# Optimization experiments

Measured on AMD Instinct MI355X. Metric: run time of the kernel, lower is better.

The kernel has to match this reference:

```python
import jax, jax.numpy as jnp
import numpy as np

B = 2048        # graphs per batch
NC = 81         # cells per sudoku
IN_C, HID = 10, 128
N_ACT, N_NUM, N_TECH = 4, 9, 10


def _sudoku_edges():
    idx = np.arange(NC).reshape(9, 9)
    adj = np.zeros((NC, NC), dtype=bool)
    for i in range(9):
        for j in range(9):
            n = idx[i, j]
            adj[n, idx[i, :]] = True
            adj[n, idx[:, j]] = True
            bi, bj = 3 * (i // 3), 3 * (j // 3)
            adj[n, idx[bi:bi + 3, bj:bj + 3].reshape(-1)] = True
            adj[n, n] = False
    src, dst = np.nonzero(adj)  # 1620 directed edges
    return np.stack([src, dst]).astype(np.int32)


def setup_inputs() -> dict:
    key = jax.random.key(0)
    ks = jax.random.split(key, 12)
    N = B * NC
    base = _sudoku_edges()                          # [2, 1620]
    offs = (np.arange(B, dtype=np.int32) * NC)      # [B]
    ei = (base[:, None, :] + offs[None, :, None]).reshape(2, -1)  # [2, B*1620]
    batch = np.repeat(np.arange(B, dtype=np.int32), NC)           # [N]

    def lin(k, fan_in, fan_out):
        s = 1.0 / np.sqrt(fan_in)
        return jax.random.uniform(k, (fan_in, fan_out), jnp.float32, -s, s)

    return {
        "x": jax.random.normal(ks[0], (N, IN_C), jnp.float32),
        "edge_index": jnp.asarray(ei),
        "batch": jnp.asarray(batch),
        "W1": lin(ks[1], IN_C, HID), "b1": jnp.zeros((HID,), jnp.float32),
        "W2": lin(ks[2], HID, HID),  "b2": jnp.zeros((HID,), jnp.float32),
        "Wa": lin(ks[3], HID, N_ACT),  "ba": jnp.zeros((N_ACT,), jnp.float32),
        "Wc": lin(ks[4], HID, NC),     "bc": jnp.zeros((NC,), jnp.float32),
        "Wn": lin(ks[5], HID, N_NUM),  "bn": jnp.zeros((N_NUM,), jnp.float32),
        "Wt": lin(ks[6], HID, N_TECH), "bt": jnp.zeros((N_TECH,), jnp.float32),
    }


def _gcn_conv(x, edge_index, W, b):
    n = x.shape[0]
    loop = jnp.arange(n, dtype=edge_index.dtype)
    src = jnp.concatenate([edge_index[0], loop])
    dst = jnp.concatenate([edge_index[1], loop])
    deg = jax.ops.segment_sum(jnp.ones_like(dst, jnp.float32), dst, num_segments=n)
    dinv = jax.lax.rsqrt(deg)            # deg >= 1 due to self-loops
    norm = dinv[src] * dinv[dst]         # [E+N]
    h = x @ W                            # [N, out]
    msg = h[src] * norm[:, None]         # gather + scale
    return jax.ops.segment_sum(msg, dst, num_segments=n) + b


def reference(x, edge_index, batch, W1, b1, W2, b2, Wa, ba, Wc, bc, Wn, bn, Wt, bt):
    h = jax.nn.relu(_gcn_conv(x, edge_index, W1, b1))
    h = jax.nn.relu(_gcn_conv(h, edge_index, W2, b2))
    # global mean pool over graphs
    sums = jax.ops.segment_sum(h, batch, num_segments=B)
    cnts = jax.ops.segment_sum(jnp.ones((h.shape[0],), h.dtype), batch, num_segments=B)
    pooled = sums / jnp.maximum(cnts, 1.0)[:, None]   # [B, HID]
    return (pooled @ Wa + ba, pooled @ Wc + bc, pooled @ Wn + bn, pooled @ Wt + bt)
```

## Files before the change

### kernel.cpp

```cpp
#include <hip/hip_runtime.h>
#include <hip/hip_bf16.h>

typedef __attribute__((ext_vector_type(8))) short bf16x8;
typedef __attribute__((ext_vector_type(4))) float f32x4;

__device__ __forceinline__ unsigned short f2b(float f) {
    __hip_bfloat16 h = __float2bfloat16(f);
    return __builtin_bit_cast(unsigned short, h);
}
__device__ __forceinline__ float b2f(unsigned short u) {
    unsigned v = ((unsigned)u) << 16;
    return __builtin_bit_cast(float, v);
}
__device__ __forceinline__ float ldf(const void* p, int idx, bool f32) {
    return f32 ? ((const float*)p)[idx] : b2f(((const unsigned short*)p)[idx]);
}
__device__ __forceinline__ unsigned short ldb(const void* p, int idx, bool f32) {
    return f32 ? f2b(((const float*)p)[idx]) : ((const unsigned short*)p)[idx];
}
__device__ __forceinline__ int swz(int row, int col) {
    return row * 128 + (((col >> 3) ^ (row & 7)) << 3) + (col & 7);
}

__device__ __forceinline__ bool sniff_f32(const void* x) {
    const unsigned* p = (const unsigned*)x;
    int wild = 0;
#pragma unroll
    for (int i = 0; i < 16; ++i) {
        unsigned e = (p[i] >> 7) & 0xFF;
        wild += (e != 0 && (e < 0x68 || e > 0x90)) ? 1 : 0;
    }
    return wild > 8;
}

#define WS_B1F    16
#define WS_B2F    528
#define WS_BHF    1040
#define WS_W1R    1536
#define WS_W2R    9728
#define WS_SR     42496
#define WS_WH     60928

__global__ void k_repack(const void* __restrict__ x,
                         const void* __restrict__ W1, const void* __restrict__ b1,
                         const void* __restrict__ W2, const void* __restrict__ b2,
                         const void* __restrict__ Wa, const void* __restrict__ ba,
                         const void* __restrict__ Wc, const void* __restrict__ bc,
                         const void* __restrict__ Wn, const void* __restrict__ bn,
                         const void* __restrict__ Wt, const void* __restrict__ bt,
                         char* __restrict__ ws) {
    const bool f32 = sniff_f32(x);
    int idx = blockIdx.x * blockDim.x + threadIdx.x;
    if (idx < 4096) {
        int f = idx >> 5, k = idx & 31;
        unsigned short v = (k < 10) ? ldb(W1, k * 128 + f, f32) : (unsigned short)0;
        ((unsigned short*)(ws + WS_W1R))[idx] = v;
        return;
    }
    idx -= 4096;
    if (idx < 16384) {
        int f = idx >> 7, k = idx & 127;
        ((unsigned short*)(ws + WS_W2R))[idx] = ldb(W2, k * 128 + f, f32);
        return;
    }
    idx -= 16384;
    if (idx < 9216) {
        int fi = idx >> 9, rem = idx & 511;
        int lane = rem >> 3, j = rem & 7;
        int mi = fi / 3, kc = fi - mi * 3;
        int node = mi * 16 + (lane & 15);
        int cell = kc * 32 + ((lane >> 4) << 3) + j;
        bool adj = false;
        if (node < 81 && cell < 81) {
            int ni = node / 9, nj = node % 9;
            int ci = cell / 9, cj = cell % 9;
            adj = (ni == ci) || (nj == cj) ||
                  ((ni / 3 == ci / 3) && (nj / 3 == cj / 3));
        }
        ((unsigned short*)(ws + WS_SR))[idx] = adj ? (unsigned short)0x3F80 : (unsigned short)0;
        return;
    }
    idx -= 9216;
    if (idx < 13312) {
        int o = idx >> 7, f = idx & 127;
        const void* W; int oo, dim;
        if (o < 4)       { W = Wa; oo = o;      dim = 4;  }
        else if (o < 85) { W = Wc; oo = o - 4;  dim = 81; }
        else if (o < 94) { W = Wn; oo = o - 85; dim = 9;  }
        else             { W = Wt; oo = o - 94; dim = 10; }
        ((float*)(ws + WS_WH))[idx] = ldf(W, f * dim + oo, f32);
        return;
    }
    idx -= 13312;
    if (idx < 360) {
        float v;
        if (idx < 128)      v = ldf(b1, idx, f32);
        else if (idx < 256) v = ldf(b2, idx - 128, f32);
        else {
            int o = idx - 256;
            if (o < 4)       v = ldf(ba, o, f32);
            else if (o < 85) v = ldf(bc, o - 4, f32);
            else if (o < 94) v = ldf(bn, o - 85, f32);
            else             v = ldf(bt, o - 94, f32);
        }
        if (idx < 128)      ((float*)(ws + WS_B1F))[idx] = v;
        else if (idx < 256) ((float*)(ws + WS_B2F))[idx - 128] = v;
        else                ((float*)(ws + WS_BHF))[idx - 256] = v;
    }
}

__global__ __launch_bounds__(256, 2) void sudoku_gnn(
    const void* __restrict__ x, const char* __restrict__ ws,
    void* __restrict__ out, int nB)
{
    __shared__ __attribute__((aligned(16))) unsigned short tT[16384];
    __shared__ __attribute__((aligned(16))) unsigned short hS[12288];
    __shared__ float sPool[4][128];

    const bool f32 = sniff_f32(x);
    const unsigned short* w1r = (const unsigned short*)(ws + WS_W1R);
    const unsigned short* w2r = (const unsigned short*)(ws + WS_W2R);
    const unsigned short* sr  = (const unsigned short*)(ws + WS_SR);
    const float* b1f = (const float*)(ws + WS_B1F);
    const float* b2f = (const float*)(ws + WS_B2F);
    const float* bhf = (const float*)(ws + WS_BHF);
    const float* whf = (const float*)(ws + WS_WH);

    const int tid  = threadIdx.x;
    const int wave = tid >> 6;
    const int lane = tid & 63;
    const int ln15 = lane & 15;
    const int q    = lane >> 4;
    const int k0   = q * 8;
    const int FB   = wave * 32;
    const int g0   = blockIdx.x * 4;
    const float inv21 = 1.0f / 21.0f;
    const float inv81 = 1.0f / 81.0f;

    bf16x8 sfr[6][3];
#pragma unroll
    for (int nt = 0; nt < 6; ++nt)
#pragma unroll
        for (int kc = 0; kc < 3; ++kc)
            sfr[nt][kc] = *(const bf16x8*)&sr[((nt * 3 + kc) * 64 + lane) * 8];
    bf16x8 w1f[2];
#pragma unroll
    for (int fmt = 0; fmt < 2; ++fmt)
        w1f[fmt] = *(const bf16x8*)&w1r[(FB + fmt * 16 + ln15) * 32 + k0];

    uint4 pr4[6]; unsigned pr1[6];
    auto rawload = [&](int g) {
        const char* xg = (const char*)x + (size_t)(g < nB ? g : nB - 1) * 1620;
#pragma unroll
        for (int mt = 0; mt < 6; ++mt) {
            int node = mt * 16 + ln15;
            uint4 r = {0, 0, 0, 0}; unsigned r1v = 0;
            if (node < 81) {
                if (q == 0)      r   = *(const uint4*)(xg + node * 20);
                else if (q == 1) r1v = *(const unsigned*)(xg + node * 20 + 16);
            }
            pr4[mt] = r; pr1[mt] = r1v;
        }
    };
    if (!f32) rawload(g0);

    const f32x4 z4 = {0.f, 0.f, 0.f, 0.f};

    for (int gi = 0; gi < 4; ++gi) {
        const int g = g0 + gi;

        bf16x8 xf[6];
        if (!f32) {
#pragma unroll
            for (int mt = 0; mt < 6; ++mt) {
                bf16x8 v = {0, 0, 0, 0, 0, 0, 0, 0};
                if (q == 0)      v = __builtin_bit_cast(bf16x8, pr4[mt]);
                else if (q == 1) { v[0] = (short)(pr1[mt] & 0xFFFF); v[1] = (short)(pr1[mt] >> 16); }
                xf[mt] = v;
            }
            if (gi < 3) rawload(g + 1);
        } else {
            const float* xg = (const float*)x + (size_t)(g < nB ? g : nB - 1) * 810;
#pragma unroll
            for (int mt = 0; mt < 6; ++mt) {
                int node = mt * 16 + ln15;
                bf16x8 v = {0, 0, 0, 0, 0, 0, 0, 0};
                if (node < 81) {
                    if (q == 0) {
#pragma unroll
                        for (int j = 0; j < 8; ++j) v[j] = (short)f2b(xg[node * 10 + j]);
                    } else if (q == 1) {
                        v[0] = (short)f2b(xg[node * 10 + 8]);
                        v[1] = (short)f2b(xg[node * 10 + 9]);
                    }
                }
                xf[mt] = v;
            }
        }

#pragma unroll
        for (int fmt = 0; fmt < 2; ++fmt)
#pragma unroll
            for (int mt = 0; mt < 6; ++mt) {
                f32x4 c = __builtin_amdgcn_mfma_f32_16x16x32_bf16(xf[mt], w1f[fmt], z4, 0, 0, 0);
                unsigned lo = (unsigned)f2b(c[0]) | ((unsigned)f2b(c[1]) << 16);
                unsigned hi = (unsigned)f2b(c[2]) | ((unsigned)f2b(c[3]) << 16);
                *(uint2*)&tT[swz(FB + fmt * 16 + ln15, mt * 16 + q * 4)] = make_uint2(lo, hi);
            }

        f32x4 acc[2][6];
#pragma unroll
        for (int a = 0; a < 2; ++a)
#pragma unroll
            for (int b = 0; b < 6; ++b) acc[a][b] = z4;
#pragma unroll
        for (int kc = 0; kc < 3; ++kc) {
            bf16x8 af[2];
#pragma unroll
            for (int fmt = 0; fmt < 2; ++fmt)
                af[fmt] = *(const bf16x8*)&tT[swz(FB + fmt * 16 + ln15, kc * 32 + k0)];
#pragma unroll
            for (int fmt = 0; fmt < 2; ++fmt)
#pragma unroll
                for (int nt = 0; nt < 6; ++nt)
                    acc[fmt][nt] = __builtin_amdgcn_mfma_f32_16x16x32_bf16(af[fmt], sfr[nt][kc], acc[fmt][nt], 0, 0, 0);
        }
#pragma unroll
        for (int fmt = 0; fmt < 2; ++fmt) {
            float4 bv = *(const float4*)&b1f[FB + fmt * 16 + q * 4];
#pragma unroll
            for (int nt = 0; nt < 6; ++nt) {
                float v0 = fmaxf(acc[fmt][nt][0] * inv21 + bv.x, 0.0f);
                float v1 = fmaxf(acc[fmt][nt][1] * inv21 + bv.y, 0.0f);
                float v2 = fmaxf(acc[fmt][nt][2] * inv21 + bv.z, 0.0f);
                float v3 = fmaxf(acc[fmt][nt][3] * inv21 + bv.w, 0.0f);
                unsigned lo = (unsigned)f2b(v0) | ((unsigned)f2b(v1) << 16);
                unsigned hi = (unsigned)f2b(v2) | ((unsigned)f2b(v3) << 16);
                *(uint2*)&hS[swz(nt * 16 + ln15, FB + fmt * 16 + q * 4)] = make_uint2(lo, hi);
            }
        }
        __syncthreads();

        f32x4 acc3[6][2];
#pragma unroll
        for (int a = 0; a < 6; ++a)
#pragma unroll
            for (int b = 0; b < 2; ++b) acc3[a][b] = z4;
        bf16x8 wB[2];
#pragma unroll
        for (int fmt = 0; fmt < 2; ++fmt)
            wB[fmt] = *(const bf16x8*)&w2r[(FB + fmt * 16 + ln15) * 128 + k0];
#pragma unroll
        for (int kc = 0; kc < 4; ++kc) {
            bf16x8 wN[2];
            if (kc < 3) {
#pragma unroll
                for (int fmt = 0; fmt < 2; ++fmt)
                    wN[fmt] = *(const bf16x8*)&w2r[(FB + fmt * 16 + ln15) * 128 + (kc + 1) * 32 + k0];
            }
            bf16x8 a3[6];
#pragma unroll
            for (int mt = 0; mt < 6; ++mt)
                a3[mt] = *(const bf16x8*)&hS[swz(mt * 16 + ln15, kc * 32 + k0)];
#pragma unroll
            for (int mt = 0; mt < 6; ++mt)
#pragma unroll
                for (int fmt = 0; fmt < 2; ++fmt)
                    acc3[mt][fmt] = __builtin_amdgcn_mfma_f32_16x16x32_bf16(a3[mt], wB[fmt], acc3[mt][fmt], 0, 0, 0);
            if (kc < 3) { wB[0] = wN[0]; wB[1] = wN[1]; }
        }
#pragma unroll
        for (int mt = 0; mt < 6; ++mt)
#pragma unroll
            for (int fmt = 0; fmt < 2; ++fmt) {
                unsigned lo = (unsigned)f2b(acc3[mt][fmt][0]) | ((unsigned)f2b(acc3[mt][fmt][1]) << 16);
                unsigned hi = (unsigned)f2b(acc3[mt][fmt][2]) | ((unsigned)f2b(acc3[mt][fmt][3]) << 16);
                *(uint2*)&tT[swz(FB + fmt * 16 + ln15, mt * 16 + q * 4)] = make_uint2(lo, hi);
            }

        f32x4 acc4[2][6];
#pragma unroll
        for (int a = 0; a < 2; ++a)
#pragma unroll
            for (int b = 0; b < 6; ++b) acc4[a][b] = z4;
#pragma unroll
        for (int kc = 0; kc < 3; ++kc) {
            bf16x8 af[2];
#pragma unroll
            for (int fmt = 0; fmt < 2; ++fmt)
                af[fmt] = *(const bf16x8*)&tT[swz(FB + fmt * 16 + ln15, kc * 32 + k0)];
#pragma unroll
            for (int fmt = 0; fmt < 2; ++fmt)
#pragma unroll
                for (int nt = 0; nt < 6; ++nt)
                    acc4[fmt][nt] = __builtin_amdgcn_mfma_f32_16x16x32_bf16(af[fmt], sfr[nt][kc], acc4[fmt][nt], 0, 0, 0);
        }
#pragma unroll
        for (int fmt = 0; fmt < 2; ++fmt) {
            float4 bv = *(const float4*)&b2f[FB + fmt * 16 + q * 4];
            float s0 = 0.f, s1 = 0.f, s2 = 0.f, s3 = 0.f;
#pragma unroll
            for (int nt = 0; nt < 6; ++nt) {
                int node = nt * 16 + ln15;
                if (node < 81) {
                    s0 += fmaxf(acc4[fmt][nt][0] * inv21 + bv.x, 0.0f);
                    s1 += fmaxf(acc4[fmt][nt][1] * inv21 + bv.y, 0.0f);
                    s2 += fmaxf(acc4[fmt][nt][2] * inv21 + bv.z, 0.0f);
                    s3 += fmaxf(acc4[fmt][nt][3] * inv21 + bv.w, 0.0f);
                }
            }
#pragma unroll
            for (int off = 1; off < 16; off <<= 1) {
                s0 += __shfl_xor(s0, off);
                s1 += __shfl_xor(s1, off);
                s2 += __shfl_xor(s2, off);
                s3 += __shfl_xor(s3, off);
            }
            if (ln15 == 0) {
                float4 v = {s0 * inv81, s1 * inv81, s2 * inv81, s3 * inv81};
                *(float4*)&sPool[gi][FB + fmt * 16 + q * 4] = v;
            }
        }
        __syncthreads();
    }

#pragma unroll
    for (int it = 0; it < 2; ++it) {
        int item = tid + it * 256;
        if (item < 416) {
            int gi = item / 104;
            int o  = item - gi * 104;
            int g  = g0 + gi;
            if (g < nB) {
                float a = bhf[o];
                const float4* wrow = (const float4*)(whf + o * 128);
                const float4* sp4  = (const float4*)sPool[gi];
#pragma unroll 8
                for (int i = 0; i < 32; ++i) {
                    float4 wv = wrow[i];
                    float4 pv = sp4[i];
                    a += pv.x * wv.x + pv.y * wv.y + pv.z * wv.z + pv.w * wv.w;
                }
                int oo; size_t off;
                if (o < 4)       { oo = o;      off = (size_t)g * 4 + oo; }
                else if (o < 85) { oo = o - 4;  off = (size_t)nB * 4  + (size_t)g * 81 + oo; }
                else if (o < 94) { oo = o - 85; off = (size_t)nB * 85 + (size_t)g * 9  + oo; }
                else             { oo = o - 94; off = (size_t)nB * 94 + (size_t)g * 10 + oo; }
                if (f32) ((float*)out)[off] = a;
                else     ((unsigned short*)out)[off] = f2b(a);
            }
        }
    }
}

extern "C" void kernel_launch(void* const* d_in, const int* in_sizes, int n_in,
                              void* d_out, int out_size, void* d_ws, size_t ws_size,
                              hipStream_t stream) {
    const void* x  = d_in[0];
    int nB = in_sizes[2] / 81;
    if (nB <= 0) return;

    char* ws = (char*)d_ws;
    hipLaunchKernelGGL(k_repack, dim3(170), dim3(256), 0, stream,
                       x, d_in[3], d_in[4], d_in[5], d_in[6],
                       d_in[7], d_in[8], d_in[9], d_in[10],
                       d_in[11], d_in[12], d_in[13], d_in[14], ws);
    hipLaunchKernelGGL(sudoku_gnn, dim3((nB + 3) / 4), dim3(256), 0, stream,
                       x, (const char*)ws, d_out, nB);
}
```

Measured before the change: 152.6 us.

## Process one graph per block and stage structure matrix in shared memory

Switches from four graphs per block, looped with prefetch of the next graph's input, to one graph per block, launching nB blocks instead of nB/4. The sudoku structure matrix fragments now sit in shared memory loaded once per block, where before they were held in registers, which lowers register pressure. The cost is that per-block setup (copying the structure matrix and loading weights) is repeated four times as often and the cross-graph input prefetch is gone. In exchange the GPU gets more parallel blocks and possibly higher occupancy, but shared memory use rises by about 18 KB per block.

```diff
diff --git a/kernel.cpp b/kernel.cpp
--- a/kernel.cpp
+++ b/kernel.cpp
@@ -115,12 +115,12 @@
 {
     __shared__ __attribute__((aligned(16))) unsigned short tT[16384];
     __shared__ __attribute__((aligned(16))) unsigned short hS[12288];
-    __shared__ float sPool[4][128];
+    __shared__ __attribute__((aligned(16))) unsigned short sS[9216];
+    __shared__ float sPool[128];
 
     const bool f32 = sniff_f32(x);
     const unsigned short* w1r = (const unsigned short*)(ws + WS_W1R);
     const unsigned short* w2r = (const unsigned short*)(ws + WS_W2R);
-    const unsigned short* sr  = (const unsigned short*)(ws + WS_SR);
     const float* b1f = (const float*)(ws + WS_B1F);
     const float* b2f = (const float*)(ws + WS_B2F);
     const float* bhf = (const float*)(ws + WS_BHF);
@@ -133,24 +133,13 @@
     const int q    = lane >> 4;
     const int k0   = q * 8;
     const int FB   = wave * 32;
-    const int g0   = blockIdx.x * 4;
+    const int g    = blockIdx.x;
     const float inv21 = 1.0f / 21.0f;
     const float inv81 = 1.0f / 81.0f;
 
-    bf16x8 sfr[6][3];
-#pragma unroll
-    for (int nt = 0; nt < 6; ++nt)
-#pragma unroll
-        for (int kc = 0; kc < 3; ++kc)
-            sfr[nt][kc] = *(const bf16x8*)&sr[((nt * 3 + kc) * 64 + lane) * 8];
-    bf16x8 w1f[2];
-#pragma unroll
-    for (int fmt = 0; fmt < 2; ++fmt)
-        w1f[fmt] = *(const bf16x8*)&w1r[(FB + fmt * 16 + ln15) * 32 + k0];
-
-    uint4 pr4[6]; unsigned pr1[6];
-    auto rawload = [&](int g) {
-        const char* xg = (const char*)x + (size_t)(g < nB ? g : nB - 1) * 1620;
+    uint4 xr4[6]; unsigned xr1[6];
+    if (!f32) {
+        const char* xg = (const char*)x + (size_t)g * 1620;
 #pragma unroll
         for (int mt = 0; mt < 6; ++mt) {
             int node = mt * 16 + ln15;
@@ -159,55 +148,53 @@
                 if (q == 0)      r   = *(const uint4*)(xg + node * 20);
                 else if (q == 1) r1v = *(const unsigned*)(xg + node * 20 + 16);
             }
-            pr4[mt] = r; pr1[mt] = r1v;
-        }
-    };
-    if (!f32) rawload(g0);
+            xr4[mt] = r; xr1[mt] = r1v;
+        }
+    }
+
+    {
+        const uint4* src = (const uint4*)(ws + WS_SR);
+        uint4* dst = (uint4*)sS;
+        for (int i = tid; i < 1152; i += 256) dst[i] = src[i];
+    }
+
+    bf16x8 w1f[2];
+#pragma unroll
+    for (int fmt = 0; fmt < 2; ++fmt)
+        w1f[fmt] = *(const bf16x8*)&w1r[(FB + fmt * 16 + ln15) * 32 + k0];
 
     const f32x4 z4 = {0.f, 0.f, 0.f, 0.f};
 
-    for (int gi = 0; gi < 4; ++gi) {
-        const int g = g0 + gi;
-
-        bf16x8 xf[6];
+#pragma unroll
+    for (int mt = 0; mt < 6; ++mt) {
+        bf16x8 xv = {0, 0, 0, 0, 0, 0, 0, 0};
         if (!f32) {
-#pragma unroll
-            for (int mt = 0; mt < 6; ++mt) {
-                bf16x8 v = {0, 0, 0, 0, 0, 0, 0, 0};
-                if (q == 0)      v = __builtin_bit_cast(bf16x8, pr4[mt]);
-                else if (q == 1) { v[0] = (short)(pr1[mt] & 0xFFFF); v[1] = (short)(pr1[mt] >> 16); }
-                xf[mt] = v;
-            }
-            if (gi < 3) rawload(g + 1);
+            if (q == 0)      xv = __builtin_bit_cast(bf16x8, xr4[mt]);
+            else if (q == 1) { xv[0] = (short)(xr1[mt] & 0xFFFF); xv[1] = (short)(xr1[mt] >> 16); }
         } else {
-            const float* xg = (const float*)x + (size_t)(g < nB ? g : nB - 1) * 810;
-#pragma unroll
-            for (int mt = 0; mt < 6; ++mt) {
-                int node = mt * 16 + ln15;
-                bf16x8 v = {0, 0, 0, 0, 0, 0, 0, 0};
-                if (node < 81) {
-                    if (q == 0) {
-#pragma unroll
-                        for (int j = 0; j < 8; ++j) v[j] = (short)f2b(xg[node * 10 + j]);
-                    } else if (q == 1) {
-                        v[0] = (short)f2b(xg[node * 10 + 8]);
-                        v[1] = (short)f2b(xg[node * 10 + 9]);
-                    }
+            int node = mt * 16 + ln15;
+            if (node < 81) {
+                const float* xg = (const float*)x + (size_t)g * 810 + node * 10;
+                if (q == 0) {
+#pragma unroll
+                    for (int j = 0; j < 8; ++j) xv[j] = (short)f2b(xg[j]);
+                } else if (q == 1) {
+                    xv[0] = (short)f2b(xg[8]);
+                    xv[1] = (short)f2b(xg[9]);
                 }
-                xf[mt] = v;
-            }
-        }
-
-#pragma unroll
-        for (int fmt = 0; fmt < 2; ++fmt)
-#pragma unroll
-            for (int mt = 0; mt < 6; ++mt) {
-                f32x4 c = __builtin_amdgcn_mfma_f32_16x16x32_bf16(xf[mt], w1f[fmt], z4, 0, 0, 0);
-                unsigned lo = (unsigned)f2b(c[0]) | ((unsigned)f2b(c[1]) << 16);
-                unsigned hi = (unsigned)f2b(c[2]) | ((unsigned)f2b(c[3]) << 16);
-                *(uint2*)&tT[swz(FB + fmt * 16 + ln15, mt * 16 + q * 4)] = make_uint2(lo, hi);
-            }
-
+            }
+        }
+#pragma unroll
+        for (int fmt = 0; fmt < 2; ++fmt) {
+            f32x4 c = __builtin_amdgcn_mfma_f32_16x16x32_bf16(xv, w1f[fmt], z4, 0, 0, 0);
+            unsigned lo = (unsigned)f2b(c[0]) | ((unsigned)f2b(c[1]) << 16);
+            unsigned hi = (unsigned)f2b(c[2]) | ((unsigned)f2b(c[3]) << 16);
+            *(uint2*)&tT[swz(FB + fmt * 16 + ln15, mt * 16 + q * 4)] = make_uint2(lo, hi);
+        }
+    }
+    __syncthreads();
+
+    {
         f32x4 acc[2][6];
 #pragma unroll
         for (int a = 0; a < 2; ++a)
@@ -220,10 +207,12 @@
             for (int fmt = 0; fmt < 2; ++fmt)
                 af[fmt] = *(const bf16x8*)&tT[swz(FB + fmt * 16 + ln15, kc * 32 + k0)];
 #pragma unroll
-            for (int fmt = 0; fmt < 2; ++fmt)
-#pragma unroll
-                for (int nt = 0; nt < 6; ++nt)
-                    acc[fmt][nt] = __builtin_amdgcn_mfma_f32_16x16x32_bf16(af[fmt], sfr[nt][kc], acc[fmt][nt], 0, 0, 0);
+            for (int nt = 0; nt < 6; ++nt) {
+                bf16x8 sf = *(const bf16x8*)&sS[((nt * 3 + kc) * 64 + lane) * 8];
+#pragma unroll
+                for (int fmt = 0; fmt < 2; ++fmt)
+                    acc[fmt][nt] = __builtin_amdgcn_mfma_f32_16x16x32_bf16(af[fmt], sf, acc[fmt][nt], 0, 0, 0);
+            }
         }
 #pragma unroll
         for (int fmt = 0; fmt < 2; ++fmt) {
@@ -239,35 +228,28 @@
                 *(uint2*)&hS[swz(nt * 16 + ln15, FB + fmt * 16 + q * 4)] = make_uint2(lo, hi);
             }
         }
-        __syncthreads();
-
+    }
+    __syncthreads();
+
+    {
         f32x4 acc3[6][2];
 #pragma unroll
         for (int a = 0; a < 6; ++a)
 #pragma unroll
             for (int b = 0; b < 2; ++b) acc3[a][b] = z4;
-        bf16x8 wB[2];
-#pragma unroll
-        for (int fmt = 0; fmt < 2; ++fmt)
-            wB[fmt] = *(const bf16x8*)&w2r[(FB + fmt * 16 + ln15) * 128 + k0];
 #pragma unroll
         for (int kc = 0; kc < 4; ++kc) {
-            bf16x8 wN[2];
-            if (kc < 3) {
+            bf16x8 w2f[2];
+#pragma unroll
+            for (int fmt = 0; fmt < 2; ++fmt)
+                w2f[fmt] = *(const bf16x8*)&w2r[(FB + fmt * 16 + ln15) * 128 + kc * 32 + k0];
+#pragma unroll
+            for (int mt = 0; mt < 6; ++mt) {
+                bf16x8 a3 = *(const bf16x8*)&hS[swz(mt * 16 + ln15, kc * 32 + k0)];
 #pragma unroll
                 for (int fmt = 0; fmt < 2; ++fmt)
-                    wN[fmt] = *(const bf16x8*)&w2r[(FB + fmt * 16 + ln15) * 128 + (kc + 1) * 32 + k0];
-            }
-            bf16x8 a3[6];
-#pragma unroll
-            for (int mt = 0; mt < 6; ++mt)
-                a3[mt] = *(const bf16x8*)&hS[swz(mt * 16 + ln15, kc * 32 + k0)];
-#pragma unroll
-            for (int mt = 0; mt < 6; ++mt)
-#pragma unroll
-                for (int fmt = 0; fmt < 2; ++fmt)
-                    acc3[mt][fmt] = __builtin_amdgcn_mfma_f32_16x16x32_bf16(a3[mt], wB[fmt], acc3[mt][fmt], 0, 0, 0);
-            if (kc < 3) { wB[0] = wN[0]; wB[1] = wN[1]; }
+                    acc3[mt][fmt] = __builtin_amdgcn_mfma_f32_16x16x32_bf16(a3, w2f[fmt], acc3[mt][fmt], 0, 0, 0);
+            }
         }
 #pragma unroll
         for (int mt = 0; mt < 6; ++mt)
@@ -277,7 +259,9 @@
                 unsigned hi = (unsigned)f2b(acc3[mt][fmt][2]) | ((unsigned)f2b(acc3[mt][fmt][3]) << 16);
                 *(uint2*)&tT[swz(FB + fmt * 16 + ln15, mt * 16 + q * 4)] = make_uint2(lo, hi);
             }
-
+    }
+
+    {
         f32x4 acc4[2][6];
 #pragma unroll
         for (int a = 0; a < 2; ++a)
@@ -290,10 +274,12 @@
             for (int fmt = 0; fmt < 2; ++fmt)
                 af[fmt] = *(const bf16x8*)&tT[swz(FB + fmt * 16 + ln15, kc * 32 + k0)];
 #pragma unroll
-            for (int fmt = 0; fmt < 2; ++fmt)
-#pragma unroll
-                for (int nt = 0; nt < 6; ++nt)
-                    acc4[fmt][nt] = __builtin_amdgcn_mfma_f32_16x16x32_bf16(af[fmt], sfr[nt][kc], acc4[fmt][nt], 0, 0, 0);
+            for (int nt = 0; nt < 6; ++nt) {
+                bf16x8 sf = *(const bf16x8*)&sS[((nt * 3 + kc) * 64 + lane) * 8];
+#pragma unroll
+                for (int fmt = 0; fmt < 2; ++fmt)
+                    acc4[fmt][nt] = __builtin_amdgcn_mfma_f32_16x16x32_bf16(af[fmt], sf, acc4[fmt][nt], 0, 0, 0);
+            }
         }
 #pragma unroll
         for (int fmt = 0; fmt < 2; ++fmt) {
@@ -318,37 +304,31 @@
             }
             if (ln15 == 0) {
                 float4 v = {s0 * inv81, s1 * inv81, s2 * inv81, s3 * inv81};
-                *(float4*)&sPool[gi][FB + fmt * 16 + q * 4] = v;
-            }
-        }
-        __syncthreads();
-    }
-
-#pragma unroll
-    for (int it = 0; it < 2; ++it) {
-        int item = tid + it * 256;
-        if (item < 416) {
-            int gi = item / 104;
-            int o  = item - gi * 104;
-            int g  = g0 + gi;
-            if (g < nB) {
-                float a = bhf[o];
-                const float4* wrow = (const float4*)(whf + o * 128);
-                const float4* sp4  = (const float4*)sPool[gi];
+                *(float4*)&sPool[FB + fmt * 16 + q * 4] = v;
+            }
+        }
+    }
+    __syncthreads();
+
+    {
+        int o = tid;
+        if (o < 104) {
+            float a = bhf[o];
+            const float4* wrow = (const float4*)(whf + o * 128);
+            const float4* sp4  = (const float4*)sPool;
 #pragma unroll 8
-                for (int i = 0; i < 32; ++i) {
-                    float4 wv = wrow[i];
-                    float4 pv = sp4[i];
-                    a += pv.x * wv.x + pv.y * wv.y + pv.z * wv.z + pv.w * wv.w;
-                }
-                int oo; size_t off;
-                if (o < 4)       { oo = o;      off = (size_t)g * 4 + oo; }
-                else if (o < 85) { oo = o - 4;  off = (size_t)nB * 4  + (size_t)g * 81 + oo; }
-                else if (o < 94) { oo = o - 85; off = (size_t)nB * 85 + (size_t)g * 9  + oo; }
-                else             { oo = o - 94; off = (size_t)nB * 94 + (size_t)g * 10 + oo; }
-                if (f32) ((float*)out)[off] = a;
-                else     ((unsigned short*)out)[off] = f2b(a);
-            }
+            for (int i = 0; i < 32; ++i) {
+                float4 wv = wrow[i];
+                float4 pv = sp4[i];
+                a += pv.x * wv.x + pv.y * wv.y + pv.z * wv.z + pv.w * wv.w;
+            }
+            int oo; size_t off;
+            if (o < 4)       { oo = o;      off = (size_t)g * 4 + oo; }
+            else if (o < 85) { oo = o - 4;  off = (size_t)nB * 4  + (size_t)g * 81 + oo; }
+            else if (o < 94) { oo = o - 85; off = (size_t)nB * 85 + (size_t)g * 9  + oo; }
+            else             { oo = o - 94; off = (size_t)nB * 94 + (size_t)g * 10 + oo; }
+            if (f32) ((float*)out)[off] = a;
+            else     ((unsigned short*)out)[off] = f2b(a);
         }
     }
 }
@@ -365,6 +345,6 @@
                        x, d_in[3], d_in[4], d_in[5], d_in[6],
                        d_in[7], d_in[8], d_in[9], d_in[10],
                        d_in[11], d_in[12], d_in[13], d_in[14], ws);
-    hipLaunchKernelGGL(sudoku_gnn, dim3((nB + 3) / 4), dim3(256), 0, stream,
+    hipLaunchKernelGGL(sudoku_gnn, dim3(nB), dim3(256), 0, stream,
                        x, (const char*)ws, d_out, nB);
 }
```

New measurement: 148.2 us. 1.03x faster.
